# Optimization experiments

Measured on AMD Instinct MI355X. Metric: run time of the kernel, lower is better.

The kernel has to match this reference:

```python
import jax, jax.numpy as jnp
import numpy as np

B, C, H, W, G = 4, 256, 64, 64, 4
K = 9  # 3x3 kernel


def _conv1x1(x, w, b):
    return jnp.einsum('bchw,oc->bohw', x, w) + b[None, :, None, None]


def _deform_conv(V, offset, mask, weight, groups):
    # torchvision modulated deform_conv2d, stride=1, pad=1, dil=1, no bias.
    Bs, Cc, Hh, Ww = V.shape
    Cg = Cc // groups
    # offset layout: [B, og, K, 2(y,x), H, W]
    off = offset.reshape(Bs, groups, K, 2, Hh, Ww)
    ky, kx = jnp.meshgrid(jnp.arange(3), jnp.arange(3), indexing='ij')
    ky = ky.reshape(K).astype(offset.dtype)
    kx = kx.reshape(K).astype(offset.dtype)
    hh = jnp.arange(Hh, dtype=offset.dtype)
    ww = jnp.arange(Ww, dtype=offset.dtype)
    # sampling positions [B, G, K, H, W]
    py = off[:, :, :, 0] + (hh[:, None] - 1.0)[None, None, None] + ky[None, None, :, None, None]
    px = off[:, :, :, 1] + (ww[None, :] - 1.0)[None, None, None] + kx[None, None, :, None, None]
    y0f = jnp.floor(py)
    x0f = jnp.floor(px)
    fy = py - y0f
    fx = px - x0f
    y0 = y0f.astype(jnp.int32)
    x0 = x0f.astype(jnp.int32)
    Vg = V.reshape(Bs, groups, Cg, Hh * Ww)

    def gather(yi, xi, wgt):
        valid = (yi >= 0) & (yi < Hh) & (xi >= 0) & (xi < Ww)
        idx = (jnp.clip(yi, 0, Hh - 1) * Ww + jnp.clip(xi, 0, Ww - 1)).reshape(Bs, groups, 1, K * Hh * Ww)
        vals = jnp.take_along_axis(Vg, jnp.broadcast_to(idx, (Bs, groups, Cg, K * Hh * Ww)), axis=3)
        vals = vals.reshape(Bs, groups, Cg, K, Hh, Ww)
        return vals * (wgt * valid.astype(wgt.dtype))[:, :, None]

    sampled = (gather(y0, x0, (1.0 - fy) * (1.0 - fx))
               + gather(y0, x0 + 1, (1.0 - fy) * fx)
               + gather(y0 + 1, x0, fy * (1.0 - fx))
               + gather(y0 + 1, x0 + 1, fy * fx))  # [B, G, Cg, K, H, W]
    m = mask.reshape(Bs, groups, K, Hh, Ww)
    wk = weight.reshape(groups, Cc // groups, Cg, K)
    out = jnp.einsum('bgikhw,bgkhw,goik->bgohw', sampled, m, wk)
    return out.reshape(Bs, Cc, Hh, Ww)


def setup_inputs() -> dict:
    key = jax.random.key(0)
    ks = jax.random.split(key, 12)
    inp = {
        'rife_feat': jax.random.normal(ks[0], (B, C, H, W), jnp.float32),
        'd0': jax.random.normal(ks[1], (B, C, H, W), jnp.float32),
        'd1': jax.random.normal(ks[2], (B, C, H, W), jnp.float32),
        'wq': jax.random.normal(ks[3], (C, C), jnp.float32) * (1.0 / np.sqrt(C)),
        'bq': jax.random.normal(ks[4], (C,), jnp.float32) * 0.01,
        'wk': jax.random.normal(ks[5], (C, C), jnp.float32) * (1.0 / np.sqrt(C)),
        'bk': jax.random.normal(ks[6], (C,), jnp.float32) * 0.01,
        'wv': jax.random.normal(ks[7], (C, C), jnp.float32) * (1.0 / np.sqrt(C)),
        'bv': jax.random.normal(ks[8], (C,), jnp.float32) * 0.01,
        'w_off': jax.random.normal(ks[9], (27 * G, 2 * C, 3, 3), jnp.float32) * 0.02,
        'b_off': jnp.zeros((27 * G,), jnp.float32),
        'dcn_w': jax.random.normal(ks[10], (C, C // G, 3, 3), jnp.float32) * 0.05,
        'gamma': jnp.ones((1,), jnp.float32),
    }
    return inp


def reference(rife_feat, d0, d1, wq, bq, wk, bk, wv, bv, w_off, b_off, dcn_w, gamma):
    Qs = jnp.concatenate([rife_feat, rife_feat], axis=0)  # [2B, C, H, W]
    Ds = jnp.concatenate([d0, d1], axis=0)
    Q = _conv1x1(Qs, wq, bq)
    Kf = _conv1x1(Ds, wk, bk)
    V = _conv1x1(Ds, wv, bv)
    comb = jnp.concatenate([Q, Kf], axis=1)  # [2B, 2C, H, W]
    out = jax.lax.conv_general_dilated(comb, w_off, (1, 1), [(1, 1), (1, 1)],
                                       dimension_numbers=('NCHW', 'OIHW', 'NCHW'))
    out = out + b_off[None, :, None, None]  # [2B, 27G, H, W]
    n = out.shape[1] // 3
    o1, o2, mlog = out[:, :n], out[:, n:2 * n], out[:, 2 * n:]
    offset = jnp.concatenate([o1, o2], axis=1)  # [2B, 18G, H, W]
    mask = jax.nn.sigmoid(mlog)
    aligned = _deform_conv(V, offset, mask, dcn_w, G)
    a0, a1 = aligned[:B], aligned[B:]
    fused = rife_feat + gamma * (a0 + a1)
    return fused, offset[:B], offset[B:]
```

## Files before the change

kernel.cpp:

```cpp
#include <hip/hip_runtime.h>
#include <math.h>

#define HW   4096
#define CDIM 256

typedef float f32x4  __attribute__((ext_vector_type(4)));
typedef short short8 __attribute__((ext_vector_type(8)));

#define FUSED_SZ (4ULL*256*HW)
#define OFF_SZ   (4ULL*72*HW)

static __device__ __forceinline__ unsigned short f2b(float f) {
    unsigned u = __float_as_uint(f);
    unsigned r = (u + 0x7fffu + ((u >> 16) & 1u)) >> 16;
    return (unsigned short)r;
}
static __device__ __forceinline__ float b2f(short h) {
    return __uint_as_float(((unsigned)(unsigned short)h) << 16);
}
static __device__ __forceinline__ unsigned pk_bf16(float a, float b) {
    unsigned r;
    asm("v_cvt_pk_bf16_f32 %0, %1, %2" : "=v"(r) : "v"(a), "v"(b));
    return r;
}
union U8 { unsigned u[4]; short8 s; };

__global__ __launch_bounds__(256) void wprep(const float* __restrict__ w_off,
                                             unsigned short* __restrict__ wT2)
{
    int idx = blockIdx.x * 256 + threadIdx.x;
    if (idx >= 9 * 128 * 512) return;
    int kk  = idx / (128 * 512);
    int rem = idx - kk * 128 * 512;
    int o = rem >> 9;
    int c = rem & 511;
    float v = (o < 108) ? w_off[((size_t)o * 512 + c) * 9 + kk] : 0.f;
    size_t flat = ((size_t)(kk * 16 + (c >> 5)) * 128 + o) * 32 + (c & 31);
    wT2[flat] = f2b(v);
}

__global__ __launch_bounds__(256) void dprep(const float* __restrict__ dcn_w,
                                             unsigned short* __restrict__ dcnwT)
{
    int idx = blockIdx.x * 256 + threadIdx.x;
    if (idx >= 9 * 256 * 64) return;
    int k   = idx / (256 * 64);
    int rem = idx - k * 256 * 64;
    int og = rem >> 6;
    int i  = rem & 63;
    int g = og >> 6, ol = og & 63;
    size_t flat = ((size_t)((k * 4 + g) * 2 + (i >> 5)) * 64 + ol) * 32 + (i & 31);
    dcnwT[flat] = f2b(dcn_w[((size_t)og * 64 + i) * 9 + k]);
}

__global__ __launch_bounds__(256) void qwprep(
    const float* __restrict__ wq, const float* __restrict__ wk,
    const float* __restrict__ wv, unsigned short* __restrict__ wqkvT)
{
    int idx = blockIdx.x * 256 + threadIdx.x;
    int o = idx >> 8;
    int c = idx & 255;
    float v = (o < 256) ? wq[(size_t)o * 256 + c]
            : (o < 512) ? wk[(size_t)(o - 256) * 256 + c]
                        : wv[(size_t)(o - 512) * 256 + c];
    wqkvT[idx] = f2b(v);
}

__global__ __launch_bounds__(256) void xprep(
    const float* __restrict__ rife, const float* __restrict__ d0,
    const float* __restrict__ d1, unsigned short* __restrict__ xT)
{
    const int pix0 = blockIdx.x * 64;
    const int img  = blockIdx.y;
    const int t    = threadIdx.x;

    const float* src = (img < 4) ? rife + (size_t)img * CDIM * HW
                     : (img < 8) ? d0 + (size_t)(img - 4) * CDIM * HW
                                 : d1 + (size_t)(img - 8) * CDIM * HW;
    unsigned short* dst = xT + (size_t)img * 4096 * 256;

    __shared__ float tile[64][65];

    for (int c0 = 0; c0 < 256; c0 += 64) {
        #pragma unroll
        for (int r = 0; r < 16; ++r) {
            int idx = t + r * 256;
            int c = idx >> 6, pp = idx & 63;
            tile[c][pp] = src[(size_t)(c0 + c) * HW + pix0 + pp];
        }
        __syncthreads();
        const int pix = t >> 2, cq = t & 3;
        const int cb = cq * 16;
        uint4 p0, p1;
        p0.x = (unsigned)f2b(tile[cb+0][pix])  | ((unsigned)f2b(tile[cb+1][pix])  << 16);
        p0.y = (unsigned)f2b(tile[cb+2][pix])  | ((unsigned)f2b(tile[cb+3][pix])  << 16);
        p0.z = (unsigned)f2b(tile[cb+4][pix])  | ((unsigned)f2b(tile[cb+5][pix])  << 16);
        p0.w = (unsigned)f2b(tile[cb+6][pix])  | ((unsigned)f2b(tile[cb+7][pix])  << 16);
        p1.x = (unsigned)f2b(tile[cb+8][pix])  | ((unsigned)f2b(tile[cb+9][pix])  << 16);
        p1.y = (unsigned)f2b(tile[cb+10][pix]) | ((unsigned)f2b(tile[cb+11][pix]) << 16);
        p1.z = (unsigned)f2b(tile[cb+12][pix]) | ((unsigned)f2b(tile[cb+13][pix]) << 16);
        p1.w = (unsigned)f2b(tile[cb+14][pix]) | ((unsigned)f2b(tile[cb+15][pix]) << 16);
        unsigned short* p = dst + (size_t)(pix0 + pix) * 256 + c0 + cb;
        *(uint4*)p = p0;
        *(uint4*)(p + 8) = p1;
        __syncthreads();
    }
}

__global__ __launch_bounds__(256) void qkv_mfma(
    const unsigned short* __restrict__ xT,
    const unsigned short* __restrict__ wqkvT,
    const float* __restrict__ bq, const float* __restrict__ bk,
    const float* __restrict__ bv,
    unsigned short* __restrict__ comb_t, unsigned short* __restrict__ vbuf_t)
{
    const int pix0 = blockIdx.x * 64;
    const int type = blockIdx.y;
    const int s    = blockIdx.z;
    const int t    = threadIdx.x;
    const int wvi  = t >> 6;
    const int lane = t & 63;
    const int q    = lane >> 4;
    const int rl   = lane & 15;

    const int img = (type == 0) ? (s & 3) : (4 + s);
    const short8* X = (const short8*)(xT + (size_t)img * 4096 * 256);
    const short8* W = (const short8*)(wqkvT + (size_t)(type * 256 + wvi * 64) * 256);
    const float* bias = (type == 0) ? bq : (type == 1) ? bk : bv;

    f32x4 acc[4][4];
    #pragma unroll
    for (int mf = 0; mf < 4; ++mf)
        #pragma unroll
        for (int nf = 0; nf < 4; ++nf)
            acc[mf][nf] = (f32x4){0.f, 0.f, 0.f, 0.f};

    #pragma unroll
    for (int c8 = 0; c8 < 32; c8 += 4) {
        short8 a[4], b[4];
        #pragma unroll
        for (int mf = 0; mf < 4; ++mf)
            a[mf] = W[(size_t)(mf * 16 + rl) * 32 + c8 + q];
        #pragma unroll
        for (int nf = 0; nf < 4; ++nf)
            b[nf] = X[(size_t)(pix0 + nf * 16 + rl) * 32 + c8 + q];
        #pragma unroll
        for (int mf = 0; mf < 4; ++mf)
            #pragma unroll
            for (int nf = 0; nf < 4; ++nf)
                acc[mf][nf] = __builtin_amdgcn_mfma_f32_16x16x32_bf16(a[mf], b[nf], acc[mf][nf], 0, 0, 0);
    }

    const int CH = (type < 2) ? 512 : 256;
    unsigned short* dst = (type < 2)
        ? comb_t + (size_t)s * 4096 * 512 + type * 256
        : vbuf_t + (size_t)s * 4096 * 256;
    #pragma unroll
    for (int mf = 0; mf < 4; ++mf) {
        const int o_loc = wvi * 64 + mf * 16 + q * 4;
        const float4 bz = *(const float4*)(bias + o_loc);
        #pragma unroll
        for (int nf = 0; nf < 4; ++nf) {
            const int pix = pix0 + nf * 16 + rl;
            uint2 pk;
            pk.x = pk_bf16(acc[mf][nf][0] + bz.x, acc[mf][nf][1] + bz.y);
            pk.y = pk_bf16(acc[mf][nf][2] + bz.z, acc[mf][nf][3] + bz.w);
            *(uint2*)(dst + (size_t)pix * CH + o_loc) = pk;
        }
    }
}

__global__ __launch_bounds__(256) void offconv_mfma(
    const unsigned short* __restrict__ comb_t,
    const unsigned short* __restrict__ wT2,
    const float* __restrict__ b_off,
    float* __restrict__ dout, float* __restrict__ mask_ws)
{
    const int bid = blockIdx.x;
    const int s = bid & 7;
    const int h = bid >> 3;
    const int t = threadIdx.x;
    const int lane = t & 63;
    const int wid  = t >> 6;
    const int q    = lane >> 4;
    const int rl   = lane & 15;

    __shared__ __align__(16) unsigned short tb[2][792 * 8];

    const short8* cbv = (const short8*)comb_t + (size_t)s * 4096 * 64;
    const short8* wv  = (const short8*)wT2;

    const int i1 = t + 256, i2 = t + 512, i3 = t + 768;

    auto sload = [&](int idx, int c8) -> short8 {
        int x = idx >> 2, cq = idx & 3;
        int ky = x / 66, xx = x - ky * 66;
        int hh = h + ky - 1, gx = xx - 1;
        short8 v = {0, 0, 0, 0, 0, 0, 0, 0};
        if (hh >= 0 && hh < 64 && gx >= 0 && gx < 64)
            v = cbv[(size_t)(hh * 64 + gx) * 64 + c8 + cq];
        return v;
    };
    auto swrite = [&](unsigned short* buf, int idx, short8 v) {
        int x = idx >> 2, cq = idx & 3;
        int qs = cq ^ ((x >> 1) & 3);
        *((short8*)buf + x * 4 + qs) = v;
    };

    f32x4 acc[2][4];
    #pragma unroll
    for (int ma = 0; ma < 2; ++ma)
        #pragma unroll
        for (int nf = 0; nf < 4; ++nf)
            acc[ma][nf] = (f32x4){0.f, 0.f, 0.f, 0.f};

    short8 r0 = sload(t, 0), r1 = sload(i1, 0), r2 = sload(i2, 0);
    short8 r3 = {0,0,0,0,0,0,0,0};
    if (i3 < 792) r3 = sload(i3, 0);
    swrite(tb[0], t, r0); swrite(tb[0], i1, r1); swrite(tb[0], i2, r2);
    if (i3 < 792) swrite(tb[0], i3, r3);
    __syncthreads();

    for (int sl = 0; sl < 16; ++sl) {
        const int c8 = sl * 4;
        if (sl < 15) {
            r0 = sload(t, c8 + 4); r1 = sload(i1, c8 + 4); r2 = sload(i2, c8 + 4);
            if (i3 < 792) r3 = sload(i3, c8 + 4);
        }
        short8 a[2][9];
        #pragma unroll
        for (int ma = 0; ma < 2; ++ma) {
            const int o = (wid * 2 + ma) * 16 + rl;
            #pragma unroll
            for (int kk = 0; kk < 9; ++kk)
                a[ma][kk] = wv[((size_t)(kk * 16 + sl) * 128 + o) * 4 + q];
        }
        const unsigned short* bufc = tb[sl & 1];
        #pragma unroll
        for (int kk = 0; kk < 9; ++kk) {
            const int ky = kk / 3, kx = kk % 3;
            #pragma unroll
            for (int nf = 0; nf < 4; ++nf) {
                const int xr = ky * 66 + nf * 16 + rl + kx;
                short8 b = *((const short8*)bufc + xr * 4 + (q ^ ((xr >> 1) & 3)));
                acc[0][nf] = __builtin_amdgcn_mfma_f32_16x16x32_bf16(a[0][kk], b, acc[0][nf], 0, 0, 0);
                acc[1][nf] = __builtin_amdgcn_mfma_f32_16x16x32_bf16(a[1][kk], b, acc[1][nf], 0, 0, 0);
            }
        }
        if (sl < 15) {
            unsigned short* bufn = tb[(sl + 1) & 1];
            swrite(bufn, t, r0); swrite(bufn, i1, r1); swrite(bufn, i2, r2);
            if (i3 < 792) swrite(bufn, i3, r3);
        }
        __syncthreads();
    }

    const size_t obase = FUSED_SZ + (s < 4 ? 0 : OFF_SZ) + (size_t)(s & 3) * 72 * HW + (size_t)h * 64;
    const size_t mbase = (size_t)s * 36 * HW + (size_t)h * 64;
    #pragma unroll
    for (int ma = 0; ma < 2; ++ma) {
        #pragma unroll
        for (int r = 0; r < 4; ++r) {
            const int o = (wid * 2 + ma) * 16 + q * 4 + r;
            if (o >= 108) continue;
            const float bz = b_off[o];
            #pragma unroll
            for (int nf = 0; nf < 4; ++nf) {
                const int w = nf * 16 + rl;
                float v = acc[ma][nf][r] + bz;
                if (o < 72)
                    dout[obase + (size_t)o * HW + w] = v;
                else
                    mask_ws[mbase + (size_t)(o - 72) * HW + w] = 1.f / (1.f + expf(-v));
            }
        }
    }
}

__global__ __launch_bounds__(256) void dcn_fuse_mfma(
    const float* __restrict__ rife, const unsigned short* __restrict__ dcnwT,
    const float* __restrict__ gamma,
    const unsigned short* __restrict__ vbuf_t, const float* __restrict__ mask_ws,
    float* __restrict__ dout)
{
    const int bid = blockIdx.x;
    const int c   = bid & 15;
    const int h   = bid >> 4;
    const int b   = c >> 2;
    const int g   = c & 3;
    const int t    = threadIdx.x;
    const int wv   = t >> 6;
    const int lane = t & 63;
    const int q    = lane >> 4;
    const int rl   = lane & 15;
    const int pix  = wv * 16 + rl;

    const short8* aT = (const short8*)dcnwT;

    f32x4 acc[4];
    #pragma unroll
    for (int ma = 0; ma < 4; ++ma) acc[ma] = (f32x4){0.f, 0.f, 0.f, 0.f};

    const size_t obA = FUSED_SZ + (size_t)b * 72 * HW + (size_t)(g * 18) * HW + (size_t)h * 64 + pix;
    const size_t obB = obA + OFF_SZ;
    const size_t mbA = (size_t)b * 36 * HW + (size_t)(g * 9) * HW + (size_t)h * 64 + pix;
    const size_t mbB = mbA + 4ULL * 36 * HW;

    auto body = [&](float pyv, float pxv, float mv, int sb, short8 (&af)[4][2]) {
        const float y0f = floorf(pyv), x0f = floorf(pxv);
        const float fy = pyv - y0f, fx = pxv - x0f;
        const int y0 = (int)y0f, x0 = (int)x0f;
        const bool vy0 = (y0 >= 0) && (y0 < 64);
        const bool vy1 = (y0 >= -1) && (y0 < 63);
        const bool vx0 = (x0 >= 0) && (x0 < 64);
        const bool vx1 = (x0 >= -1) && (x0 < 63);
        const float w00 = (1.f - fy) * (1.f - fx) * mv * (float)(vy0 && vx0);
        const float w01 = (1.f - fy) * fx        * mv * (float)(vy0 && vx1);
        const float w10 = fy * (1.f - fx)        * mv * (float)(vy1 && vx0);
        const float w11 = fy * fx                * mv * (float)(vy1 && vx1);
        const int yc0 = min(max(y0, 0), 63),     yc1 = min(max(y0 + 1, 0), 63);
        const int xc0 = min(max(x0, 0), 63),     xc1 = min(max(x0 + 1, 0), 63);
        const size_t o00 = (size_t)(yc0 * 64 + xc0) * 256;
        const size_t o01 = (size_t)(yc0 * 64 + xc1) * 256;
        const size_t o10 = (size_t)(yc1 * 64 + xc0) * 256;
        const size_t o11 = (size_t)(yc1 * 64 + xc1) * 256;

        const unsigned short* Vb = vbuf_t + (size_t)sb * 4096 * 256 + g * 64 + q * 8;

        short8 v00a = *(const short8*)(Vb + o00);
        short8 v01a = *(const short8*)(Vb + o01);
        short8 v10a = *(const short8*)(Vb + o10);
        short8 v11a = *(const short8*)(Vb + o11);
        short8 v00b = *(const short8*)(Vb + o00 + 32);
        short8 v01b = *(const short8*)(Vb + o01 + 32);
        short8 v10b = *(const short8*)(Vb + o10 + 32);
        short8 v11b = *(const short8*)(Vb + o11 + 32);

        U8 u0, u1;
        #pragma unroll
        for (int j = 0; j < 4; ++j) {
            const int ce = 2 * j, co = 2 * j + 1;
            float e0 = w00 * b2f(v00a[ce]) + w01 * b2f(v01a[ce])
                     + w10 * b2f(v10a[ce]) + w11 * b2f(v11a[ce]);
            float e1 = w00 * b2f(v00a[co]) + w01 * b2f(v01a[co])
                     + w10 * b2f(v10a[co]) + w11 * b2f(v11a[co]);
            u0.u[j] = pk_bf16(e0, e1);
            float f0 = w00 * b2f(v00b[ce]) + w01 * b2f(v01b[ce])
                     + w10 * b2f(v10b[ce]) + w11 * b2f(v11b[ce]);
            float f1 = w00 * b2f(v00b[co]) + w01 * b2f(v01b[co])
                     + w10 * b2f(v10b[co]) + w11 * b2f(v11b[co]);
            u1.u[j] = pk_bf16(f0, f1);
        }
        short8 bf0 = u0.s, bf1 = u1.s;
        acc[0] = __builtin_amdgcn_mfma_f32_16x16x32_bf16(af[0][0], bf0, acc[0], 0, 0, 0);
        acc[1] = __builtin_amdgcn_mfma_f32_16x16x32_bf16(af[1][0], bf0, acc[1], 0, 0, 0);
        acc[2] = __builtin_amdgcn_mfma_f32_16x16x32_bf16(af[2][0], bf0, acc[2], 0, 0, 0);
        acc[3] = __builtin_amdgcn_mfma_f32_16x16x32_bf16(af[3][0], bf0, acc[3], 0, 0, 0);
        acc[0] = __builtin_amdgcn_mfma_f32_16x16x32_bf16(af[0][1], bf1, acc[0], 0, 0, 0);
        acc[1] = __builtin_amdgcn_mfma_f32_16x16x32_bf16(af[1][1], bf1, acc[1], 0, 0, 0);
        acc[2] = __builtin_amdgcn_mfma_f32_16x16x32_bf16(af[2][1], bf1, acc[2], 0, 0, 0);
        acc[3] = __builtin_amdgcn_mfma_f32_16x16x32_bf16(af[3][1], bf1, acc[3], 0, 0, 0);
    };

    float cyA = dout[obA],      cxA = dout[obA + HW],      cmA = mask_ws[mbA];
    float cyB = dout[obB],      cxB = dout[obB + HW],      cmB = mask_ws[mbB];

    #pragma unroll
    for (int k = 0; k < 9; ++k) {
        const int ky = k / 3, kx = k % 3;
        short8 af[4][2];
        #pragma unroll
        for (int ma = 0; ma < 4; ++ma)
            #pragma unroll
            for (int ks = 0; ks < 2; ++ks)
                af[ma][ks] = aT[((size_t)((k * 4 + g) * 2 + ks) * 64 + ma * 16 + rl) * 4 + q];
        float nyA = 0.f, nxA = 0.f, nmA = 0.f, nyB = 0.f, nxB = 0.f, nmB = 0.f;
        if (k < 8) {
            nyA = dout[obA + (size_t)((k + 1) * 2) * HW];
            nxA = dout[obA + (size_t)((k + 1) * 2 + 1) * HW];
            nmA = mask_ws[mbA + (size_t)(k + 1) * HW];
            nyB = dout[obB + (size_t)((k + 1) * 2) * HW];
            nxB = dout[obB + (size_t)((k + 1) * 2 + 1) * HW];
            nmB = mask_ws[mbB + (size_t)(k + 1) * HW];
        }
        body(cyA + (float)(h - 1 + ky), cxA + (float)(pix - 1 + kx), cmA, b,     af);
        body(cyB + (float)(h - 1 + ky), cxB + (float)(pix - 1 + kx), cmB, b + 4, af);
        if (k < 8) { cyA = nyA; cxA = nxA; cmA = nmA; cyB = nyB; cxB = nxB; cmB = nmB; }
    }

    const float gm = gamma[0];
    #pragma unroll
    for (int ma = 0; ma < 4; ++ma) {
        #pragma unroll
        for (int r = 0; r < 4; ++r) {
            const int o = g * 64 + ma * 16 + q * 4 + r;
            const size_t addr = ((size_t)b * 256 + o) * HW + (size_t)h * 64 + pix;
            dout[addr] = rife[addr] + gm * acc[ma][r];
        }
    }
}

extern "C" void kernel_launch(void* const* d_in, const int* in_sizes, int n_in,
                              void* d_out, int out_size, void* d_ws, size_t ws_size,
                              hipStream_t stream)
{
    const float* rife  = (const float*)d_in[0];
    const float* d0    = (const float*)d_in[1];
    const float* d1    = (const float*)d_in[2];
    const float* wq    = (const float*)d_in[3];
    const float* bq    = (const float*)d_in[4];
    const float* wk    = (const float*)d_in[5];
    const float* bk    = (const float*)d_in[6];
    const float* wv    = (const float*)d_in[7];
    const float* bv    = (const float*)d_in[8];
    const float* w_off = (const float*)d_in[9];
    const float* b_off = (const float*)d_in[10];
    const float* dcnw  = (const float*)d_in[11];
    const float* gamma = (const float*)d_in[12];
    float* out = (float*)d_out;
    char* wsb  = (char*)d_ws;

    unsigned short* comb_t = (unsigned short*)(wsb);
    unsigned short* vbuf_t = (unsigned short*)(wsb + 33554432);
    float*          mws    = (float*)(wsb + 50331648);
    unsigned short* wT2    = (unsigned short*)(wsb + 55050240);
    unsigned short* dcnwT  = (unsigned short*)(wsb + 56229888);
    unsigned short* xT     = (unsigned short*)(wsb + 56524800);
    unsigned short* wqkvT  = (unsigned short*)(wsb + 81690624);

    wprep<<<2304, 256, 0, stream>>>(w_off, wT2);
    dprep<<<576, 256, 0, stream>>>(dcnw, dcnwT);
    qwprep<<<768, 256, 0, stream>>>(wq, wk, wv, wqkvT);
    xprep<<<dim3(64, 12), 256, 0, stream>>>(rife, d0, d1, xT);
    qkv_mfma<<<dim3(64, 3, 8), 256, 0, stream>>>(xT, wqkvT, bq, bk, bv, comb_t, vbuf_t);
    offconv_mfma<<<512, 256, 0, stream>>>(comb_t, wT2, b_off, out, mws);
    dcn_fuse_mfma<<<1024, 256, 0, stream>>>(rife, dcnwT, gamma, vbuf_t, mws, out);
}
```

Baseline: 215.6 us.

## Merge weight prep kernels, split offconv rows, batch DCN gathers, packed bf16 convert

Three weight-prep kernels are merged into one launch to cut launch overhead. The offset conv now splits each row into two 32-pixel halves, doubling the grid to 1024 blocks with a smaller LDS tile and fewer accumulators. The DCN kernel issues all 16 bilinear gathers for both images up front before blending, to expose more memory-level parallelism, and adds an occupancy hint of 4 blocks per SM via launch bounds. xprep uses the hardware packed bf16 conversion. Risks include more register pressure from the batched gathers and extra halo reloads in offconv.

```diff
diff --git a/kernel.cpp b/kernel.cpp
--- a/kernel.cpp
+++ b/kernel.cpp
@@ -25,45 +25,43 @@
 }
 union U8 { unsigned u[4]; short8 s; };
 
-__global__ __launch_bounds__(256) void wprep(const float* __restrict__ w_off,
-                                             unsigned short* __restrict__ wT2)
-{
-    int idx = blockIdx.x * 256 + threadIdx.x;
-    if (idx >= 9 * 128 * 512) return;
-    int kk  = idx / (128 * 512);
-    int rem = idx - kk * 128 * 512;
-    int o = rem >> 9;
-    int c = rem & 511;
-    float v = (o < 108) ? w_off[((size_t)o * 512 + c) * 9 + kk] : 0.f;
-    size_t flat = ((size_t)(kk * 16 + (c >> 5)) * 128 + o) * 32 + (c & 31);
-    wT2[flat] = f2b(v);
-}
-
-__global__ __launch_bounds__(256) void dprep(const float* __restrict__ dcn_w,
-                                             unsigned short* __restrict__ dcnwT)
-{
-    int idx = blockIdx.x * 256 + threadIdx.x;
-    if (idx >= 9 * 256 * 64) return;
-    int k   = idx / (256 * 64);
-    int rem = idx - k * 256 * 64;
-    int og = rem >> 6;
-    int i  = rem & 63;
-    int g = og >> 6, ol = og & 63;
-    size_t flat = ((size_t)((k * 4 + g) * 2 + (i >> 5)) * 64 + ol) * 32 + (i & 31);
-    dcnwT[flat] = f2b(dcn_w[((size_t)og * 64 + i) * 9 + k]);
-}
-
-__global__ __launch_bounds__(256) void qwprep(
+__global__ __launch_bounds__(256) void prep_all(
+    const float* __restrict__ w_off, const float* __restrict__ dcn_w,
     const float* __restrict__ wq, const float* __restrict__ wk,
-    const float* __restrict__ wv, unsigned short* __restrict__ wqkvT)
-{
-    int idx = blockIdx.x * 256 + threadIdx.x;
-    int o = idx >> 8;
-    int c = idx & 255;
-    float v = (o < 256) ? wq[(size_t)o * 256 + c]
-            : (o < 512) ? wk[(size_t)(o - 256) * 256 + c]
-                        : wv[(size_t)(o - 512) * 256 + c];
-    wqkvT[idx] = f2b(v);
+    const float* __restrict__ wv,
+    unsigned short* __restrict__ wT2, unsigned short* __restrict__ dcnwT,
+    unsigned short* __restrict__ wqkvT)
+{
+    const int bid = blockIdx.x;
+    if (bid < 2304) {
+        int idx = bid * 256 + threadIdx.x;
+        int kk  = idx / (128 * 512);
+        int rem = idx - kk * 128 * 512;
+        int o = rem >> 9;
+        int c = rem & 511;
+        float v = (o < 108) ? w_off[((size_t)o * 512 + c) * 9 + kk] : 0.f;
+        size_t flat = ((size_t)(kk * 16 + (c >> 5)) * 128 + o) * 32 + (c & 31);
+        wT2[flat] = f2b(v);
+    } else if (bid < 2880) {
+        int idx = (bid - 2304) * 256 + threadIdx.x;
+        if (idx < 9 * 256 * 64) {
+            int k   = idx / (256 * 64);
+            int rem = idx - k * 256 * 64;
+            int og = rem >> 6;
+            int i  = rem & 63;
+            int g = og >> 6, ol = og & 63;
+            size_t flat = ((size_t)((k * 4 + g) * 2 + (i >> 5)) * 64 + ol) * 32 + (i & 31);
+            dcnwT[flat] = f2b(dcn_w[((size_t)og * 64 + i) * 9 + k]);
+        }
+    } else {
+        int idx = (bid - 2880) * 256 + threadIdx.x;
+        int o = idx >> 8;
+        int c = idx & 255;
+        float v = (o < 256) ? wq[(size_t)o * 256 + c]
+                : (o < 512) ? wk[(size_t)(o - 256) * 256 + c]
+                            : wv[(size_t)(o - 512) * 256 + c];
+        wqkvT[idx] = f2b(v);
+    }
 }
 
 __global__ __launch_bounds__(256) void xprep(
@@ -92,14 +90,14 @@
         const int pix = t >> 2, cq = t & 3;
         const int cb = cq * 16;
         uint4 p0, p1;
-        p0.x = (unsigned)f2b(tile[cb+0][pix])  | ((unsigned)f2b(tile[cb+1][pix])  << 16);
-        p0.y = (unsigned)f2b(tile[cb+2][pix])  | ((unsigned)f2b(tile[cb+3][pix])  << 16);
-        p0.z = (unsigned)f2b(tile[cb+4][pix])  | ((unsigned)f2b(tile[cb+5][pix])  << 16);
-        p0.w = (unsigned)f2b(tile[cb+6][pix])  | ((unsigned)f2b(tile[cb+7][pix])  << 16);
-        p1.x = (unsigned)f2b(tile[cb+8][pix])  | ((unsigned)f2b(tile[cb+9][pix])  << 16);
-        p1.y = (unsigned)f2b(tile[cb+10][pix]) | ((unsigned)f2b(tile[cb+11][pix]) << 16);
-        p1.z = (unsigned)f2b(tile[cb+12][pix]) | ((unsigned)f2b(tile[cb+13][pix]) << 16);
-        p1.w = (unsigned)f2b(tile[cb+14][pix]) | ((unsigned)f2b(tile[cb+15][pix]) << 16);
+        p0.x = pk_bf16(tile[cb+0][pix],  tile[cb+1][pix]);
+        p0.y = pk_bf16(tile[cb+2][pix],  tile[cb+3][pix]);
+        p0.z = pk_bf16(tile[cb+4][pix],  tile[cb+5][pix]);
+        p0.w = pk_bf16(tile[cb+6][pix],  tile[cb+7][pix]);
+        p1.x = pk_bf16(tile[cb+8][pix],  tile[cb+9][pix]);
+        p1.y = pk_bf16(tile[cb+10][pix], tile[cb+11][pix]);
+        p1.z = pk_bf16(tile[cb+12][pix], tile[cb+13][pix]);
+        p1.w = pk_bf16(tile[cb+14][pix], tile[cb+15][pix]);
         unsigned short* p = dst + (size_t)(pix0 + pix) * 256 + c0 + cb;
         *(uint4*)p = p0;
         *(uint4*)(p + 8) = p1;
@@ -177,25 +175,25 @@
     float* __restrict__ dout, float* __restrict__ mask_ws)
 {
     const int bid = blockIdx.x;
-    const int s = bid & 7;
-    const int h = bid >> 3;
+    const int s   = bid & 7;
+    const int hw2 = bid >> 3;
+    const int wz  = hw2 & 1;
+    const int h   = hw2 >> 1;
     const int t = threadIdx.x;
     const int lane = t & 63;
     const int wid  = t >> 6;
     const int q    = lane >> 4;
     const int rl   = lane & 15;
 
-    __shared__ __align__(16) unsigned short tb[2][792 * 8];
+    __shared__ __align__(16) unsigned short tb[2][408 * 8];
 
     const short8* cbv = (const short8*)comb_t + (size_t)s * 4096 * 64;
     const short8* wv  = (const short8*)wT2;
 
-    const int i1 = t + 256, i2 = t + 512, i3 = t + 768;
-
     auto sload = [&](int idx, int c8) -> short8 {
         int x = idx >> 2, cq = idx & 3;
-        int ky = x / 66, xx = x - ky * 66;
-        int hh = h + ky - 1, gx = xx - 1;
+        int ky = x / 34, xx = x - ky * 34;
+        int hh = h + ky - 1, gx = wz * 32 + xx - 1;
         short8 v = {0, 0, 0, 0, 0, 0, 0, 0};
         if (hh >= 0 && hh < 64 && gx >= 0 && gx < 64)
             v = cbv[(size_t)(hh * 64 + gx) * 64 + c8 + cq];
@@ -207,25 +205,26 @@
         *((short8*)buf + x * 4 + qs) = v;
     };
 
-    f32x4 acc[2][4];
+    f32x4 acc[2][2];
     #pragma unroll
     for (int ma = 0; ma < 2; ++ma)
         #pragma unroll
-        for (int nf = 0; nf < 4; ++nf)
+        for (int nf = 0; nf < 2; ++nf)
             acc[ma][nf] = (f32x4){0.f, 0.f, 0.f, 0.f};
 
-    short8 r0 = sload(t, 0), r1 = sload(i1, 0), r2 = sload(i2, 0);
-    short8 r3 = {0,0,0,0,0,0,0,0};
-    if (i3 < 792) r3 = sload(i3, 0);
-    swrite(tb[0], t, r0); swrite(tb[0], i1, r1); swrite(tb[0], i2, r2);
-    if (i3 < 792) swrite(tb[0], i3, r3);
+    const int i1 = t + 256;
+    short8 r0 = sload(t, 0);
+    short8 r1 = {0,0,0,0,0,0,0,0};
+    if (i1 < 408) r1 = sload(i1, 0);
+    swrite(tb[0], t, r0);
+    if (i1 < 408) swrite(tb[0], i1, r1);
     __syncthreads();
 
     for (int sl = 0; sl < 16; ++sl) {
         const int c8 = sl * 4;
         if (sl < 15) {
-            r0 = sload(t, c8 + 4); r1 = sload(i1, c8 + 4); r2 = sload(i2, c8 + 4);
-            if (i3 < 792) r3 = sload(i3, c8 + 4);
+            r0 = sload(t, c8 + 4);
+            if (i1 < 408) r1 = sload(i1, c8 + 4);
         }
         short8 a[2][9];
         #pragma unroll
@@ -240,8 +239,8 @@
         for (int kk = 0; kk < 9; ++kk) {
             const int ky = kk / 3, kx = kk % 3;
             #pragma unroll
-            for (int nf = 0; nf < 4; ++nf) {
-                const int xr = ky * 66 + nf * 16 + rl + kx;
+            for (int nf = 0; nf < 2; ++nf) {
+                const int xr = ky * 34 + nf * 16 + rl + kx;
                 short8 b = *((const short8*)bufc + xr * 4 + (q ^ ((xr >> 1) & 3)));
                 acc[0][nf] = __builtin_amdgcn_mfma_f32_16x16x32_bf16(a[0][kk], b, acc[0][nf], 0, 0, 0);
                 acc[1][nf] = __builtin_amdgcn_mfma_f32_16x16x32_bf16(a[1][kk], b, acc[1][nf], 0, 0, 0);
@@ -249,8 +248,8 @@
         }
         if (sl < 15) {
             unsigned short* bufn = tb[(sl + 1) & 1];
-            swrite(bufn, t, r0); swrite(bufn, i1, r1); swrite(bufn, i2, r2);
-            if (i3 < 792) swrite(bufn, i3, r3);
+            swrite(bufn, t, r0);
+            if (i1 < 408) swrite(bufn, i1, r1);
         }
         __syncthreads();
     }
@@ -265,8 +264,8 @@
             if (o >= 108) continue;
             const float bz = b_off[o];
             #pragma unroll
-            for (int nf = 0; nf < 4; ++nf) {
-                const int w = nf * 16 + rl;
+            for (int nf = 0; nf < 2; ++nf) {
+                const int w = wz * 32 + nf * 16 + rl;
                 float v = acc[ma][nf][r] + bz;
                 if (o < 72)
                     dout[obase + (size_t)o * HW + w] = v;
@@ -277,7 +276,7 @@
     }
 }
 
-__global__ __launch_bounds__(256) void dcn_fuse_mfma(
+__global__ __launch_bounds__(256, 4) void dcn_fuse_mfma(
     const float* __restrict__ rife, const unsigned short* __restrict__ dcnwT,
     const float* __restrict__ gamma,
     const unsigned short* __restrict__ vbuf_t, const float* __restrict__ mask_ws,
@@ -306,86 +305,140 @@
     const size_t mbA = (size_t)b * 36 * HW + (size_t)(g * 9) * HW + (size_t)h * 64 + pix;
     const size_t mbB = mbA + 4ULL * 36 * HW;
 
-    auto body = [&](float pyv, float pxv, float mv, int sb, short8 (&af)[4][2]) {
-        const float y0f = floorf(pyv), x0f = floorf(pxv);
-        const float fy = pyv - y0f, fx = pxv - x0f;
+    const unsigned short* VbA = vbuf_t + (size_t)b * 4096 * 256 + g * 64 + q * 8;
+    const unsigned short* VbB = VbA + 4ULL * 4096 * 256;
+
+    auto bil = [&](float py, float px, float mv,
+                   float& w00, float& w01, float& w10, float& w11,
+                   size_t& o00, size_t& o01, size_t& o10, size_t& o11) {
+        const float y0f = floorf(py), x0f = floorf(px);
+        const float fy = py - y0f, fx = px - x0f;
         const int y0 = (int)y0f, x0 = (int)x0f;
         const bool vy0 = (y0 >= 0) && (y0 < 64);
         const bool vy1 = (y0 >= -1) && (y0 < 63);
         const bool vx0 = (x0 >= 0) && (x0 < 64);
         const bool vx1 = (x0 >= -1) && (x0 < 63);
-        const float w00 = (1.f - fy) * (1.f - fx) * mv * (float)(vy0 && vx0);
-        const float w01 = (1.f - fy) * fx        * mv * (float)(vy0 && vx1);
-        const float w10 = fy * (1.f - fx)        * mv * (float)(vy1 && vx0);
-        const float w11 = fy * fx                * mv * (float)(vy1 && vx1);
+        w00 = (1.f - fy) * (1.f - fx) * mv * (float)(vy0 && vx0);
+        w01 = (1.f - fy) * fx        * mv * (float)(vy0 && vx1);
+        w10 = fy * (1.f - fx)        * mv * (float)(vy1 && vx0);
+        w11 = fy * fx                * mv * (float)(vy1 && vx1);
         const int yc0 = min(max(y0, 0), 63),     yc1 = min(max(y0 + 1, 0), 63);
         const int xc0 = min(max(x0, 0), 63),     xc1 = min(max(x0 + 1, 0), 63);
-        const size_t o00 = (size_t)(yc0 * 64 + xc0) * 256;
-        const size_t o01 = (size_t)(yc0 * 64 + xc1) * 256;
-        const size_t o10 = (size_t)(yc1 * 64 + xc0) * 256;
-        const size_t o11 = (size_t)(yc1 * 64 + xc1) * 256;
-
-        const unsigned short* Vb = vbuf_t + (size_t)sb * 4096 * 256 + g * 64 + q * 8;
-
-        short8 v00a = *(const short8*)(Vb + o00);
-        short8 v01a = *(const short8*)(Vb + o01);
-        short8 v10a = *(const short8*)(Vb + o10);
-        short8 v11a = *(const short8*)(Vb + o11);
-        short8 v00b = *(const short8*)(Vb + o00 + 32);
-        short8 v01b = *(const short8*)(Vb + o01 + 32);
-        short8 v10b = *(const short8*)(Vb + o10 + 32);
-        short8 v11b = *(const short8*)(Vb + o11 + 32);
-
+        o00 = (size_t)(yc0 * 64 + xc0) * 256;
+        o01 = (size_t)(yc0 * 64 + xc1) * 256;
+        o10 = (size_t)(yc1 * 64 + xc0) * 256;
+        o11 = (size_t)(yc1 * 64 + xc1) * 256;
+    };
+    auto blend = [&](short8 c00a, short8 c01a, short8 c10a, short8 c11a,
+                     short8 c00b, short8 c01b, short8 c10b, short8 c11b,
+                     float w00, float w01, float w10, float w11,
+                     short8& bf0, short8& bf1) {
         U8 u0, u1;
         #pragma unroll
         for (int j = 0; j < 4; ++j) {
             const int ce = 2 * j, co = 2 * j + 1;
-            float e0 = w00 * b2f(v00a[ce]) + w01 * b2f(v01a[ce])
-                     + w10 * b2f(v10a[ce]) + w11 * b2f(v11a[ce]);
-            float e1 = w00 * b2f(v00a[co]) + w01 * b2f(v01a[co])
-                     + w10 * b2f(v10a[co]) + w11 * b2f(v11a[co]);
+            float e0 = w00 * b2f(c00a[ce]) + w01 * b2f(c01a[ce])
+                     + w10 * b2f(c10a[ce]) + w11 * b2f(c11a[ce]);
+            float e1 = w00 * b2f(c00a[co]) + w01 * b2f(c01a[co])
+                     + w10 * b2f(c10a[co]) + w11 * b2f(c11a[co]);
             u0.u[j] = pk_bf16(e0, e1);
-            float f0 = w00 * b2f(v00b[ce]) + w01 * b2f(v01b[ce])
-                     + w10 * b2f(v10b[ce]) + w11 * b2f(v11b[ce]);
-            float f1 = w00 * b2f(v00b[co]) + w01 * b2f(v01b[co])
-                     + w10 * b2f(v10b[co]) + w11 * b2f(v11b[co]);
+            float f0 = w00 * b2f(c00b[ce]) + w01 * b2f(c01b[ce])
+                     + w10 * b2f(c10b[ce]) + w11 * b2f(c11b[ce]);
+            float f1 = w00 * b2f(c00b[co]) + w01 * b2f(c01b[co])
+                     + w10 * b2f(c10b[co]) + w11 * b2f(c11b[co]);
             u1.u[j] = pk_bf16(f0, f1);
         }
-        short8 bf0 = u0.s, bf1 = u1.s;
-        acc[0] = __builtin_amdgcn_mfma_f32_16x16x32_bf16(af[0][0], bf0, acc[0], 0, 0, 0);
-        acc[1] = __builtin_amdgcn_mfma_f32_16x16x32_bf16(af[1][0], bf0, acc[1], 0, 0, 0);
-        acc[2] = __builtin_amdgcn_mfma_f32_16x16x32_bf16(af[2][0], bf0, acc[2], 0, 0, 0);
-        acc[3] = __builtin_amdgcn_mfma_f32_16x16x32_bf16(af[3][0], bf0, acc[3], 0, 0, 0);
-        acc[0] = __builtin_amdgcn_mfma_f32_16x16x32_bf16(af[0][1], bf1, acc[0], 0, 0, 0);
-        acc[1] = __builtin_amdgcn_mfma_f32_16x16x32_bf16(af[1][1], bf1, acc[1], 0, 0, 0);
-        acc[2] = __builtin_amdgcn_mfma_f32_16x16x32_bf16(af[2][1], bf1, acc[2], 0, 0, 0);
-        acc[3] = __builtin_amdgcn_mfma_f32_16x16x32_bf16(af[3][1], bf1, acc[3], 0, 0, 0);
+        bf0 = u0.s; bf1 = u1.s;
     };
 
-    float cyA = dout[obA],      cxA = dout[obA + HW],      cmA = mask_ws[mbA];
-    float cyB = dout[obB],      cxB = dout[obB + HW],      cmB = mask_ws[mbB];
-
-    #pragma unroll
+    float cyA = dout[obA], cxA = dout[obA + HW], cmA = mask_ws[mbA];
+    float cyB = dout[obB], cxB = dout[obB + HW], cmB = mask_ws[mbB];
+
     for (int k = 0; k < 9; ++k) {
-        const int ky = k / 3, kx = k % 3;
+        const int ky = k / 3, kx = k - ky * 3;
         short8 af[4][2];
         #pragma unroll
         for (int ma = 0; ma < 4; ++ma)
             #pragma unroll
             for (int ks = 0; ks < 2; ++ks)
                 af[ma][ks] = aT[((size_t)((k * 4 + g) * 2 + ks) * 64 + ma * 16 + rl) * 4 + q];
-        float nyA = 0.f, nxA = 0.f, nmA = 0.f, nyB = 0.f, nxB = 0.f, nmB = 0.f;
+
+        float wA00, wA01, wA10, wA11, wB00, wB01, wB10, wB11;
+        size_t oA00, oA01, oA10, oA11, oB00, oB01, oB10, oB11;
+        bil(cyA + (float)(h - 1 + ky), cxA + (float)(pix - 1 + kx), cmA,
+            wA00, wA01, wA10, wA11, oA00, oA01, oA10, oA11);
+        bil(cyB + (float)(h - 1 + ky), cxB + (float)(pix - 1 + kx), cmB,
+            wB00, wB01, wB10, wB11, oB00, oB01, oB10, oB11);
+
+        short8 A00a = *(const short8*)(VbA + oA00);
+        short8 A01a = *(const short8*)(VbA + oA01);
+        short8 A10a = *(const short8*)(VbA + oA10);
+        short8 A11a = *(const short8*)(VbA + oA11);
+        short8 A00b = *(const short8*)(VbA + oA00 + 32);
+        short8 A01b = *(const short8*)(VbA + oA01 + 32);
+        short8 A10b = *(const short8*)(VbA + oA10 + 32);
+        short8 A11b = *(const short8*)(VbA + oA11 + 32);
+        short8 B00a = *(const short8*)(VbB + oB00);
+        short8 B01a = *(const short8*)(VbB + oB01);
+        short8 B10a = *(const short8*)(VbB + oB10);
+        short8 B11a = *(const short8*)(VbB + oB11);
+        short8 B00b = *(const short8*)(VbB + oB00 + 32);
+        short8 B01b = *(const short8*)(VbB + oB01 + 32);
+        short8 B10b = *(const short8*)(VbB + oB10 + 32);
+        short8 B11b = *(const short8*)(VbB + oB11 + 32);
+
         if (k < 8) {
-            nyA = dout[obA + (size_t)((k + 1) * 2) * HW];
-            nxA = dout[obA + (size_t)((k + 1) * 2 + 1) * HW];
-            nmA = mask_ws[mbA + (size_t)(k + 1) * HW];
-            nyB = dout[obB + (size_t)((k + 1) * 2) * HW];
-            nxB = dout[obB + (size_t)((k + 1) * 2 + 1) * HW];
-            nmB = mask_ws[mbB + (size_t)(k + 1) * HW];
-        }
-        body(cyA + (float)(h - 1 + ky), cxA + (float)(pix - 1 + kx), cmA, b,     af);
-        body(cyB + (float)(h - 1 + ky), cxB + (float)(pix - 1 + kx), cmB, b + 4, af);
-        if (k < 8) { cyA = nyA; cxA = nxA; cmA = nmA; cyB = nyB; cxB = nxB; cmB = nmB; }
+            float nyA = dout[obA + (size_t)((k + 1) * 2) * HW];
+            float nxA = dout[obA + (size_t)((k + 1) * 2 + 1) * HW];
+            float nmA = mask_ws[mbA + (size_t)(k + 1) * HW];
+            float nyB = dout[obB + (size_t)((k + 1) * 2) * HW];
+            float nxB = dout[obB + (size_t)((k + 1) * 2 + 1) * HW];
+            float nmB = mask_ws[mbB + (size_t)(k + 1) * HW];
+            short8 bf0, bf1;
+            blend(A00a, A01a, A10a, A11a, A00b, A01b, A10b, A11b,
+                  wA00, wA01, wA10, wA11, bf0, bf1);
+            acc[0] = __builtin_amdgcn_mfma_f32_16x16x32_bf16(af[0][0], bf0, acc[0], 0, 0, 0);
+            acc[1] = __builtin_amdgcn_mfma_f32_16x16x32_bf16(af[1][0], bf0, acc[1], 0, 0, 0);
+            acc[2] = __builtin_amdgcn_mfma_f32_16x16x32_bf16(af[2][0], bf0, acc[2], 0, 0, 0);
+            acc[3] = __builtin_amdgcn_mfma_f32_16x16x32_bf16(af[3][0], bf0, acc[3], 0, 0, 0);
+            acc[0] = __builtin_amdgcn_mfma_f32_16x16x32_bf16(af[0][1], bf1, acc[0], 0, 0, 0);
+            acc[1] = __builtin_amdgcn_mfma_f32_16x16x32_bf16(af[1][1], bf1, acc[1], 0, 0, 0);
+            acc[2] = __builtin_amdgcn_mfma_f32_16x16x32_bf16(af[2][1], bf1, acc[2], 0, 0, 0);
+            acc[3] = __builtin_amdgcn_mfma_f32_16x16x32_bf16(af[3][1], bf1, acc[3], 0, 0, 0);
+            blend(B00a, B01a, B10a, B11a, B00b, B01b, B10b, B11b,
+                  wB00, wB01, wB10, wB11, bf0, bf1);
+            acc[0] = __builtin_amdgcn_mfma_f32_16x16x32_bf16(af[0][0], bf0, acc[0], 0, 0, 0);
+            acc[1] = __builtin_amdgcn_mfma_f32_16x16x32_bf16(af[1][0], bf0, acc[1], 0, 0, 0);
+            acc[2] = __builtin_amdgcn_mfma_f32_16x16x32_bf16(af[2][0], bf0, acc[2], 0, 0, 0);
+            acc[3] = __builtin_amdgcn_mfma_f32_16x16x32_bf16(af[3][0], bf0, acc[3], 0, 0, 0);
+            acc[0] = __builtin_amdgcn_mfma_f32_16x16x32_bf16(af[0][1], bf1, acc[0], 0, 0, 0);
+            acc[1] = __builtin_amdgcn_mfma_f32_16x16x32_bf16(af[1][1], bf1, acc[1], 0, 0, 0);
+            acc[2] = __builtin_amdgcn_mfma_f32_16x16x32_bf16(af[2][1], bf1, acc[2], 0, 0, 0);
+            acc[3] = __builtin_amdgcn_mfma_f32_16x16x32_bf16(af[3][1], bf1, acc[3], 0, 0, 0);
+            cyA = nyA; cxA = nxA; cmA = nmA; cyB = nyB; cxB = nxB; cmB = nmB;
+        } else {
+            short8 bf0, bf1;
+            blend(A00a, A01a, A10a, A11a, A00b, A01b, A10b, A11b,
+                  wA00, wA01, wA10, wA11, bf0, bf1);
+            acc[0] = __builtin_amdgcn_mfma_f32_16x16x32_bf16(af[0][0], bf0, acc[0], 0, 0, 0);
+            acc[1] = __builtin_amdgcn_mfma_f32_16x16x32_bf16(af[1][0], bf0, acc[1], 0, 0, 0);
+            acc[2] = __builtin_amdgcn_mfma_f32_16x16x32_bf16(af[2][0], bf0, acc[2], 0, 0, 0);
+            acc[3] = __builtin_amdgcn_mfma_f32_16x16x32_bf16(af[3][0], bf0, acc[3], 0, 0, 0);
+            acc[0] = __builtin_amdgcn_mfma_f32_16x16x32_bf16(af[0][1], bf1, acc[0], 0, 0, 0);
+            acc[1] = __builtin_amdgcn_mfma_f32_16x16x32_bf16(af[1][1], bf1, acc[1], 0, 0, 0);
+            acc[2] = __builtin_amdgcn_mfma_f32_16x16x32_bf16(af[2][1], bf1, acc[2], 0, 0, 0);
+            acc[3] = __builtin_amdgcn_mfma_f32_16x16x32_bf16(af[3][1], bf1, acc[3], 0, 0, 0);
+            blend(B00a, B01a, B10a, B11a, B00b, B01b, B10b, B11b,
+                  wB00, wB01, wB10, wB11, bf0, bf1);
+            acc[0] = __builtin_amdgcn_mfma_f32_16x16x32_bf16(af[0][0], bf0, acc[0], 0, 0, 0);
+            acc[1] = __builtin_amdgcn_mfma_f32_16x16x32_bf16(af[1][0], bf0, acc[1], 0, 0, 0);
+            acc[2] = __builtin_amdgcn_mfma_f32_16x16x32_bf16(af[2][0], bf0, acc[2], 0, 0, 0);
+            acc[3] = __builtin_amdgcn_mfma_f32_16x16x32_bf16(af[3][0], bf0, acc[3], 0, 0, 0);
+            acc[0] = __builtin_amdgcn_mfma_f32_16x16x32_bf16(af[0][1], bf1, acc[0], 0, 0, 0);
+            acc[1] = __builtin_amdgcn_mfma_f32_16x16x32_bf16(af[1][1], bf1, acc[1], 0, 0, 0);
+            acc[2] = __builtin_amdgcn_mfma_f32_16x16x32_bf16(af[2][1], bf1, acc[2], 0, 0, 0);
+            acc[3] = __builtin_amdgcn_mfma_f32_16x16x32_bf16(af[3][1], bf1, acc[3], 0, 0, 0);
+        }
     }
 
     const float gm = gamma[0];
@@ -428,11 +481,9 @@
     unsigned short* xT     = (unsigned short*)(wsb + 56524800);
     unsigned short* wqkvT  = (unsigned short*)(wsb + 81690624);
 
-    wprep<<<2304, 256, 0, stream>>>(w_off, wT2);
-    dprep<<<576, 256, 0, stream>>>(dcnw, dcnwT);
-    qwprep<<<768, 256, 0, stream>>>(wq, wk, wv, wqkvT);
+    prep_all<<<3648, 256, 0, stream>>>(w_off, dcnw, wq, wk, wv, wT2, dcnwT, wqkvT);
     xprep<<<dim3(64, 12), 256, 0, stream>>>(rife, d0, d1, xT);
     qkv_mfma<<<dim3(64, 3, 8), 256, 0, stream>>>(xT, wqkvT, bq, bk, bv, comb_t, vbuf_t);
-    offconv_mfma<<<512, 256, 0, stream>>>(comb_t, wT2, b_off, out, mws);
+    offconv_mfma<<<1024, 256, 0, stream>>>(comb_t, wT2, b_off, out, mws);
     dcn_fuse_mfma<<<1024, 256, 0, stream>>>(rife, dcnwT, gamma, vbuf_t, mws, out);
 }
```

After: 309.9 us. 43.8% more time.
